# Kernel tuning notes

Measured on AMD Instinct MI355X. Metric: run time of the kernel, lower is better.

## Reference

```python
import jax, jax.numpy as jnp
import numpy as np

N_NODES = 100000
N_EDGES = 1600000
N_GRAPHS = 64
NUM_FEATURES = 512
NUM_CLASSES = 10


def setup_inputs() -> dict:
    key = jax.random.key(0)
    ks = jax.random.split(key, 8)
    x = jax.random.normal(ks[0], (N_NODES, NUM_FEATURES), dtype=jnp.float32)
    edge_index = jax.random.randint(ks[1], (2, N_EDGES), 0, N_NODES, dtype=jnp.int32)
    batch = jnp.sort(jax.random.randint(ks[2], (N_NODES,), 0, N_GRAPHS, dtype=jnp.int32))
    def init_w(k, fin, fout):
        return jax.random.normal(k, (fin, fout), dtype=jnp.float32) * (1.0 / np.sqrt(fin))
    W1 = init_w(ks[3], NUM_FEATURES, 128)
    W2 = init_w(ks[4], 128, 64)
    W3 = init_w(ks[5], 64, 32)
    Wfc = init_w(ks[6], 32, NUM_CLASSES)
    return {
        "x": x, "edge_index": edge_index, "batch": batch,
        "W1": W1, "b1": jnp.zeros((128,), jnp.float32),
        "W2": W2, "b2": jnp.zeros((64,), jnp.float32),
        "W3": W3, "b3": jnp.zeros((32,), jnp.float32),
        "Wfc": Wfc, "bfc": jnp.zeros((NUM_CLASSES,), jnp.float32),
    }


def _gcn_conv(x, src, dst, norm, W, b):
    # PyG GCNConv: linear first, then normalized neighbor aggregation (with self-loops), then bias.
    h = x @ W                                   # [N, F_out]
    msg = norm[:, None] * h[src]                # gather + scale, [E+N, F_out]
    out = jnp.zeros_like(h).at[dst].add(msg)    # scatter-add to targets
    return out + b


def reference(x, edge_index, batch, W1, b1, W2, b2, W3, b3, Wfc, bfc):
    n = x.shape[0]
    loops = jnp.arange(n, dtype=edge_index.dtype)
    src = jnp.concatenate([edge_index[0], loops])  # source nodes (+ self-loops)
    dst = jnp.concatenate([edge_index[1], loops])  # target nodes (+ self-loops)
    # symmetric normalization D^{-1/2} (A+I) D^{-1/2}; degrees counted at targets
    deg = jnp.zeros((n,), x.dtype).at[dst].add(1.0)
    dinv = jnp.where(deg > 0, jax.lax.rsqrt(deg), 0.0)
    norm = dinv[src] * dinv[dst]                # [E+N]

    h = jax.nn.relu(_gcn_conv(x, src, dst, norm, W1, b1))   # dropout is identity in eval
    h = jax.nn.relu(_gcn_conv(h, src, dst, norm, W2, b2))
    h = jax.nn.relu(_gcn_conv(h, src, dst, norm, W3, b3))

    pooled = jax.ops.segment_max(h, batch, num_segments=N_GRAPHS)  # global max pool per graph
    logits = pooled @ Wfc + bfc
    return jax.nn.log_softmax(logits, axis=1)
```

## Files before the change

### kernel.cpp

```cpp
#include <hip/hip_runtime.h>
#include <hip/hip_bf16.h>


typedef __attribute__((ext_vector_type(8))) short short8;
typedef __attribute__((ext_vector_type(8))) unsigned short ushort8v;
typedef __attribute__((ext_vector_type(4))) float f32x4;

__device__ __forceinline__ unsigned short f2bf(float f) {
    __hip_bfloat16 h = __float2bfloat16(f);
    return *(unsigned short*)&h;
}
__device__ __forceinline__ float bfu2f(unsigned short u) {
    unsigned int v = ((unsigned int)u) << 16;
    return __uint_as_float(v);
}

__global__ void init_kernel(int* __restrict__ cnt, float* __restrict__ pooled, int N) {
    int i = blockIdx.x * 256 + threadIdx.x;
    if (i < N) cnt[i] = 0;
    if (i < 64 * 32) pooled[i] = 0.0f;
}

__global__ void fill_slab(const int* __restrict__ src, const int* __restrict__ dst,
                          int* __restrict__ cnt, int* __restrict__ slab, int E) {
    int e = blockIdx.x * 256 + threadIdx.x;
    if (e < E) {
        int d = dst[e];
        int pos = atomicAdd(&cnt[d], 1);
        if (pos < 64) slab[(size_t)d * 64 + pos] = src[e];
    }
}

__global__ void dinv_kernel(const int* __restrict__ cnt, float* __restrict__ dinv, int N) {
    int i = blockIdx.x * 256 + threadIdx.x;
    if (i < N) dinv[i] = rsqrtf(1.0f + (float)cnt[i]);
}

__global__ void wconv(const float* __restrict__ W, unsigned short* __restrict__ Wt,
                      int K, int N) {
    int idx = blockIdx.x * 256 + threadIdx.x;
    if (idx < N * K) {
        int n = idx / K, k = idx % K;
        Wt[idx] = f2bf(W[(size_t)k * N + n]);
    }
}

template <int NOUT, bool A_BF16>
__global__ __launch_bounds__(256) void mfma_gemm(
        const float* __restrict__ Af, const unsigned short* __restrict__ Ab,
        const unsigned short* __restrict__ Wt, const float* __restrict__ dinv,
        unsigned short* __restrict__ C, int M, int K) {
    constexpr int NT = NOUT / 16;
    constexpr int CH = 136;

    __shared__ short As[16 * CH];
    __shared__ short Bs[NT * 4 * CH];

    const int t = threadIdx.x;
    const int w = t >> 6;
    const int lane = t & 63;
    const int row0 = blockIdx.x * 64;

    f32x4 acc[NT];
#pragma unroll
    for (int c = 0; c < NT; ++c) acc[c] = (f32x4){0.f, 0.f, 0.f, 0.f};

    const int ar = t >> 2;
    const int aq = t & 3;
    const int arow = row0 + ar;
    const int a_lds = ((ar >> 4) * 4 + aq) * CH + (ar & 15) * 8;

    const int bn = t >> 1;
    const int bh = t & 1;
    const int b_lds0 = ((bn >> 4) * 4 + 2 * bh) * CH + (bn & 15) * 8;

    for (int k0 = 0; k0 < K; k0 += 32) {
        short8 apack;
        if (A_BF16) {
            if (arow < M) apack = *(const short8*)&Ab[(size_t)arow * K + k0 + aq * 8];
            else apack = (short8){0, 0, 0, 0, 0, 0, 0, 0};
        } else {
            float4 u0 = make_float4(0.f, 0.f, 0.f, 0.f), u1 = u0;
            if (arow < M) {
                const float* ap = Af + (size_t)arow * K + k0 + aq * 8;
                u0 = *(const float4*)ap;
                u1 = *(const float4*)(ap + 4);
            }
            apack[0] = (short)f2bf(u0.x); apack[1] = (short)f2bf(u0.y);
            apack[2] = (short)f2bf(u0.z); apack[3] = (short)f2bf(u0.w);
            apack[4] = (short)f2bf(u1.x); apack[5] = (short)f2bf(u1.y);
            apack[6] = (short)f2bf(u1.z); apack[7] = (short)f2bf(u1.w);
        }
        short8 w0, w1;
        if (t < 2 * NOUT) {
            const unsigned short* wp = Wt + (size_t)bn * K + k0 + 16 * bh;
            w0 = *(const short8*)wp;
            w1 = *(const short8*)(wp + 8);
        }
        __syncthreads();
        *(short8*)&As[a_lds] = apack;
        if (t < 2 * NOUT) {
            *(short8*)&Bs[b_lds0] = w0;
            *(short8*)&Bs[b_lds0 + CH] = w1;
        }
        __syncthreads();

        short8 a = *(short8*)&As[(w * 4 + (lane >> 4)) * CH + (lane & 15) * 8];
#pragma unroll
        for (int c = 0; c < NT; ++c) {
            short8 b = *(short8*)&Bs[(c * 4 + (lane >> 4)) * CH + (lane & 15) * 8];
            acc[c] = __builtin_amdgcn_mfma_f32_16x16x32_bf16(a, b, acc[c], 0, 0, 0);
        }
    }

    const int q = lane >> 4, i = lane & 15;
#pragma unroll
    for (int reg = 0; reg < 4; ++reg) {
        int row = row0 + w * 16 + q * 4 + reg;
        if (row < M) {
            float di = dinv[row];
#pragma unroll
            for (int c = 0; c < NT; ++c)
                C[(size_t)row * NOUT + c * 16 + i] = f2bf(di * acc[c][reg]);
        }
    }
}

template <int F, bool OUT_BF16>
__global__ void gather_relu(const int* __restrict__ cnt, const int* __restrict__ slab,
                            const float* __restrict__ dinv,
                            const unsigned short* __restrict__ hs,
                            const float* __restrict__ bias, void* __restrict__ outv, int N) {
    constexpr int F8 = F / 8;
    constexpr int NPB = 256 / F8;
    const int node = blockIdx.x * NPB + threadIdx.x / F8;
    if (node >= N) return;
    const int lane = threadIdx.x % F8;
    const size_t fo = (size_t)lane * 8;

    float acc[8];
    {
        ushort8v s = *(const ushort8v*)&hs[(size_t)node * F + fo];
#pragma unroll
        for (int i = 0; i < 8; ++i) acc[i] = bfu2f(s[i]);
    }
    const int deg = cnt[node];
    const int* sl = slab + (size_t)node * 64;

    int j = 0;
    for (; j + 4 <= deg; j += 4) {
        int4 s4 = *(const int4*)&sl[j];
        ushort8v v0 = *(const ushort8v*)&hs[(size_t)s4.x * F + fo];
        ushort8v v1 = *(const ushort8v*)&hs[(size_t)s4.y * F + fo];
        ushort8v v2 = *(const ushort8v*)&hs[(size_t)s4.z * F + fo];
        ushort8v v3 = *(const ushort8v*)&hs[(size_t)s4.w * F + fo];
#pragma unroll
        for (int i = 0; i < 8; ++i)
            acc[i] += (bfu2f(v0[i]) + bfu2f(v1[i])) + (bfu2f(v2[i]) + bfu2f(v3[i]));
    }
    for (; j < deg; ++j) {
        int s = sl[j];
        ushort8v v = *(const ushort8v*)&hs[(size_t)s * F + fo];
#pragma unroll
        for (int i = 0; i < 8; ++i) acc[i] += bfu2f(v[i]);
    }

    const float di = dinv[node];
    if (OUT_BF16) {
        ushort8v o;
#pragma unroll
        for (int i = 0; i < 8; ++i) o[i] = f2bf(fmaxf(di * acc[i] + bias[fo + i], 0.f));
        *(ushort8v*)&((unsigned short*)outv)[(size_t)node * F + fo] = o;
    } else {
        float ov[8];
#pragma unroll
        for (int i = 0; i < 8; ++i) ov[i] = fmaxf(di * acc[i] + bias[fo + i], 0.f);
        float4* op = (float4*)&((float*)outv)[(size_t)node * F + fo];
        op[0] = make_float4(ov[0], ov[1], ov[2], ov[3]);
        op[1] = make_float4(ov[4], ov[5], ov[6], ov[7]);
    }
}

__global__ void pool_max(const float* __restrict__ h, const int* __restrict__ batch,
                         float* __restrict__ pooled, int N) {
    int t = blockIdx.x * 256 + threadIdx.x;
    int f = t % 32;
    int i0 = (t / 32) * 32;
    if (i0 >= N) return;
    int gcur = -1;
    float vmax = 0.f;
    for (int j = 0; j < 32; ++j) {
        int i = i0 + j;
        if (i >= N) break;
        int g = batch[i];
        if (g != gcur) {
            if (gcur >= 0) atomicMax((int*)&pooled[gcur * 32 + f], __float_as_int(vmax));
            gcur = g;
            vmax = 0.f;
        }
        vmax = fmaxf(vmax, h[(size_t)i * 32 + f]);
    }
    if (gcur >= 0) atomicMax((int*)&pooled[gcur * 32 + f], __float_as_int(vmax));
}

__global__ void head_kernel(const float* __restrict__ pooled, const float* __restrict__ Wfc,
                            const float* __restrict__ bfc, float* __restrict__ out) {
    int g = threadIdx.x;
    float p[32];
#pragma unroll
    for (int f = 0; f < 32; ++f) p[f] = pooled[g * 32 + f];
    float logits[10];
#pragma unroll
    for (int c = 0; c < 10; ++c) {
        float acc = bfc[c];
#pragma unroll
        for (int f = 0; f < 32; ++f) acc += p[f] * Wfc[f * 10 + c];
        logits[c] = acc;
    }
    float m = logits[0];
#pragma unroll
    for (int c = 1; c < 10; ++c) m = fmaxf(m, logits[c]);
    float s = 0.f;
#pragma unroll
    for (int c = 0; c < 10; ++c) s += expf(logits[c] - m);
    float lse = m + logf(s);
#pragma unroll
    for (int c = 0; c < 10; ++c) out[g * 10 + c] = logits[c] - lse;
}

extern "C" void kernel_launch(void* const* d_in, const int* in_sizes, int n_in,
                              void* d_out, int out_size, void* d_ws, size_t ws_size,
                              hipStream_t stream) {
    const float* x   = (const float*)d_in[0];
    const int*   ei  = (const int*)d_in[1];
    const int*   bat = (const int*)d_in[2];
    const float* W1  = (const float*)d_in[3];
    const float* b1  = (const float*)d_in[4];
    const float* W2  = (const float*)d_in[5];
    const float* b2  = (const float*)d_in[6];
    const float* W3  = (const float*)d_in[7];
    const float* b3  = (const float*)d_in[8];
    const float* Wfc = (const float*)d_in[9];
    const float* bfc = (const float*)d_in[10];
    float* out = (float*)d_out;

    const int N = in_sizes[2];
    const int E = in_sizes[1] / 2;
    const int K0 = in_sizes[0] / N;

    const int* src = ei;
    const int* dst = ei + E;

    float* ws = (float*)d_ws;
    float* dinv = ws;
    unsigned short* HS  = (unsigned short*)(ws + N);
    unsigned short* ACT = HS + (size_t)N * 128;
    float* H3 = (float*)ACT;
    float* pooled = (float*)(ACT + (size_t)N * 128);
    unsigned short* Wt1 = (unsigned short*)(pooled + 2048);
    unsigned short* Wt2 = Wt1 + 128 * 512;
    unsigned short* Wt3 = Wt2 + 64 * 128;
    int* iws = (int*)(Wt3 + 32 * 64);
    int* cnt = iws;
    int* slab = cnt + N;

    const int nb = (N + 255) / 256;
    const int eb = (E + 255) / 256;
    const int gb = (N + 63) / 64;

    init_kernel<<<nb, 256, 0, stream>>>(cnt, pooled, N);
    fill_slab<<<eb, 256, 0, stream>>>(src, dst, cnt, slab, E);
    dinv_kernel<<<nb, 256, 0, stream>>>(cnt, dinv, N);

    wconv<<<(128 * 512 + 255) / 256, 256, 0, stream>>>(W1, Wt1, K0, 128);
    wconv<<<(64 * 128 + 255) / 256, 256, 0, stream>>>(W2, Wt2, 128, 64);
    wconv<<<(32 * 64 + 255) / 256, 256, 0, stream>>>(W3, Wt3, 64, 32);

    const int gath128 = (N + 15) / 16;
    const int gath64  = (N + 31) / 32;
    const int gath32  = (N + 63) / 64;

    mfma_gemm<128, false><<<gb, 256, 0, stream>>>(x, nullptr, Wt1, dinv, HS, N, K0);
    gather_relu<128, true><<<gath128, 256, 0, stream>>>(cnt, slab, dinv, HS, b1, ACT, N);

    mfma_gemm<64, true><<<gb, 256, 0, stream>>>(nullptr, ACT, Wt2, dinv, HS, N, 128);
    gather_relu<64, true><<<gath64, 256, 0, stream>>>(cnt, slab, dinv, HS, b2, ACT, N);

    mfma_gemm<32, true><<<gb, 256, 0, stream>>>(nullptr, ACT, Wt3, dinv, HS, N, 64);
    gather_relu<32, false><<<gath32, 256, 0, stream>>>(cnt, slab, dinv, HS, b3, H3, N);

    pool_max<<<(((N + 31) / 32) * 32 + 255) / 256, 256, 0, stream>>>(H3, bat, pooled, N);
    head_kernel<<<1, 64, 0, stream>>>(pooled, Wfc, bfc, out);
}
```

Baseline: 603.5 us.

## Overlap first GEMM with edge slab fill in one interleaved launch

Merges the layer-1 GEMM and the edge bucketing (atomic slab fill) into a single kernel whose blocks alternate between GEMM and fill work. The two are independent, so the memory-bound GEMM and the atomic-heavy fill can run concurrently. Because dinv is not yet known when the GEMM runs, layer-1 normalization moves into the first gather, which now reads dinv per neighbour. The gather also gains an 8-wide unrolled loop and clamps degree to 64. The cost is extra dinv loads and multiplies in the layer-1 gather and some block-scheduling imbalance between the two kinds of work.

```diff
diff --git a/kernel.cpp b/kernel.cpp
--- a/kernel.cpp
+++ b/kernel.cpp
@@ -19,16 +19,6 @@
     int i = blockIdx.x * 256 + threadIdx.x;
     if (i < N) cnt[i] = 0;
     if (i < 64 * 32) pooled[i] = 0.0f;
-}
-
-__global__ void fill_slab(const int* __restrict__ src, const int* __restrict__ dst,
-                          int* __restrict__ cnt, int* __restrict__ slab, int E) {
-    int e = blockIdx.x * 256 + threadIdx.x;
-    if (e < E) {
-        int d = dst[e];
-        int pos = atomicAdd(&cnt[d], 1);
-        if (pos < 64) slab[(size_t)d * 64 + pos] = src[e];
-    }
 }
 
 __global__ void dinv_kernel(const int* __restrict__ cnt, float* __restrict__ dinv, int N) {
@@ -45,8 +35,9 @@
     }
 }
 
-template <int NOUT, bool A_BF16>
-__global__ __launch_bounds__(256) void mfma_gemm(
+template <int NOUT, bool A_BF16, bool SCALE>
+__device__ __forceinline__ void gemm_body(
+        int bid,
         const float* __restrict__ Af, const unsigned short* __restrict__ Ab,
         const unsigned short* __restrict__ Wt, const float* __restrict__ dinv,
         unsigned short* __restrict__ C, int M, int K) {
@@ -59,7 +50,7 @@
     const int t = threadIdx.x;
     const int w = t >> 6;
     const int lane = t & 63;
-    const int row0 = blockIdx.x * 64;
+    const int row0 = bid * 64;
 
     f32x4 acc[NT];
 #pragma unroll
@@ -118,7 +109,7 @@
     for (int reg = 0; reg < 4; ++reg) {
         int row = row0 + w * 16 + q * 4 + reg;
         if (row < M) {
-            float di = dinv[row];
+            float di = SCALE ? dinv[row] : 1.0f;
 #pragma unroll
             for (int c = 0; c < NT; ++c)
                 C[(size_t)row * NOUT + c * 16 + i] = f2bf(di * acc[c][reg]);
@@ -126,7 +117,57 @@
     }
 }
 
-template <int F, bool OUT_BF16>
+template <int NOUT, bool A_BF16>
+__global__ __launch_bounds__(256) void mfma_gemm(
+        const float* __restrict__ Af, const unsigned short* __restrict__ Ab,
+        const unsigned short* __restrict__ Wt, const float* __restrict__ dinv,
+        unsigned short* __restrict__ C, int M, int K) {
+    gemm_body<NOUT, A_BF16, true>(blockIdx.x, Af, Ab, Wt, dinv, C, M, K);
+}
+
+__global__ __launch_bounds__(256) void gemm1_fill(
+        const float* __restrict__ x, const unsigned short* __restrict__ Wt,
+        unsigned short* __restrict__ C, int M, int K,
+        const int* __restrict__ src, const int* __restrict__ dst,
+        int* __restrict__ cnt, int* __restrict__ slab, int E,
+        int gb, int fb) {
+    const int bx = blockIdx.x;
+    const int m = gb < fb ? gb : fb;
+    bool isg;
+    int bid;
+    if (bx < 2 * m) {
+        isg = (bx & 1) == 0;
+        bid = bx >> 1;
+    } else {
+        bid = bx - m;
+        isg = (gb > fb);
+    }
+    if (isg) {
+        gemm_body<128, false, false>(bid, x, nullptr, Wt, nullptr, C, M, K);
+    } else {
+        int e0 = bid * 1024 + (int)threadIdx.x * 4;
+        if (e0 + 4 <= E) {
+            int d0 = dst[e0], d1 = dst[e0 + 1], d2 = dst[e0 + 2], d3 = dst[e0 + 3];
+            int s0 = src[e0], s1 = src[e0 + 1], s2 = src[e0 + 2], s3 = src[e0 + 3];
+            int p0 = atomicAdd(&cnt[d0], 1);
+            int p1 = atomicAdd(&cnt[d1], 1);
+            int p2 = atomicAdd(&cnt[d2], 1);
+            int p3 = atomicAdd(&cnt[d3], 1);
+            if (p0 < 64) slab[(size_t)d0 * 64 + p0] = s0;
+            if (p1 < 64) slab[(size_t)d1 * 64 + p1] = s1;
+            if (p2 < 64) slab[(size_t)d2 * 64 + p2] = s2;
+            if (p3 < 64) slab[(size_t)d3 * 64 + p3] = s3;
+        } else {
+            for (int e = e0; e < E; ++e) {
+                int d = dst[e];
+                int p = atomicAdd(&cnt[d], 1);
+                if (p < 64) slab[(size_t)d * 64 + p] = src[e];
+            }
+        }
+    }
+}
+
+template <int F, bool OUT_BF16, bool PRESCALED>
 __global__ void gather_relu(const int* __restrict__ cnt, const int* __restrict__ slab,
                             const float* __restrict__ dinv,
                             const unsigned short* __restrict__ hs,
@@ -137,35 +178,76 @@
     if (node >= N) return;
     const int lane = threadIdx.x % F8;
     const size_t fo = (size_t)lane * 8;
+    const float di = dinv[node];
 
     float acc[8];
     {
         ushort8v s = *(const ushort8v*)&hs[(size_t)node * F + fo];
 #pragma unroll
-        for (int i = 0; i < 8; ++i) acc[i] = bfu2f(s[i]);
-    }
-    const int deg = cnt[node];
+        for (int i = 0; i < 8; ++i) acc[i] = PRESCALED ? bfu2f(s[i]) : di * bfu2f(s[i]);
+    }
+    int deg = cnt[node];
+    if (deg > 64) deg = 64;
     const int* sl = slab + (size_t)node * 64;
 
     int j = 0;
+    for (; j + 8 <= deg; j += 8) {
+        int4 a4 = *(const int4*)&sl[j];
+        int4 b4 = *(const int4*)&sl[j + 4];
+        ushort8v v0 = *(const ushort8v*)&hs[(size_t)a4.x * F + fo];
+        ushort8v v1 = *(const ushort8v*)&hs[(size_t)a4.y * F + fo];
+        ushort8v v2 = *(const ushort8v*)&hs[(size_t)a4.z * F + fo];
+        ushort8v v3 = *(const ushort8v*)&hs[(size_t)a4.w * F + fo];
+        ushort8v v4 = *(const ushort8v*)&hs[(size_t)b4.x * F + fo];
+        ushort8v v5 = *(const ushort8v*)&hs[(size_t)b4.y * F + fo];
+        ushort8v v6 = *(const ushort8v*)&hs[(size_t)b4.z * F + fo];
+        ushort8v v7 = *(const ushort8v*)&hs[(size_t)b4.w * F + fo];
+        if (PRESCALED) {
+#pragma unroll
+            for (int i = 0; i < 8; ++i)
+                acc[i] += ((bfu2f(v0[i]) + bfu2f(v1[i])) + (bfu2f(v2[i]) + bfu2f(v3[i]))) +
+                          ((bfu2f(v4[i]) + bfu2f(v5[i])) + (bfu2f(v6[i]) + bfu2f(v7[i])));
+        } else {
+            float w0 = dinv[a4.x], w1 = dinv[a4.y], w2 = dinv[a4.z], w3 = dinv[a4.w];
+            float w4 = dinv[b4.x], w5 = dinv[b4.y], w6 = dinv[b4.z], w7 = dinv[b4.w];
+#pragma unroll
+            for (int i = 0; i < 8; ++i) {
+                float s01 = fmaf(w0, bfu2f(v0[i]), w1 * bfu2f(v1[i]));
+                float s23 = fmaf(w2, bfu2f(v2[i]), w3 * bfu2f(v3[i]));
+                float s45 = fmaf(w4, bfu2f(v4[i]), w5 * bfu2f(v5[i]));
+                float s67 = fmaf(w6, bfu2f(v6[i]), w7 * bfu2f(v7[i]));
+                acc[i] += (s01 + s23) + (s45 + s67);
+            }
+        }
+    }
     for (; j + 4 <= deg; j += 4) {
         int4 s4 = *(const int4*)&sl[j];
         ushort8v v0 = *(const ushort8v*)&hs[(size_t)s4.x * F + fo];
         ushort8v v1 = *(const ushort8v*)&hs[(size_t)s4.y * F + fo];
         ushort8v v2 = *(const ushort8v*)&hs[(size_t)s4.z * F + fo];
         ushort8v v3 = *(const ushort8v*)&hs[(size_t)s4.w * F + fo];
-#pragma unroll
-        for (int i = 0; i < 8; ++i)
-            acc[i] += (bfu2f(v0[i]) + bfu2f(v1[i])) + (bfu2f(v2[i]) + bfu2f(v3[i]));
+        if (PRESCALED) {
+#pragma unroll
+            for (int i = 0; i < 8; ++i)
+                acc[i] += (bfu2f(v0[i]) + bfu2f(v1[i])) + (bfu2f(v2[i]) + bfu2f(v3[i]));
+        } else {
+            float w0 = dinv[s4.x], w1 = dinv[s4.y], w2 = dinv[s4.z], w3 = dinv[s4.w];
+#pragma unroll
+            for (int i = 0; i < 8; ++i) {
+                float s01 = fmaf(w0, bfu2f(v0[i]), w1 * bfu2f(v1[i]));
+                float s23 = fmaf(w2, bfu2f(v2[i]), w3 * bfu2f(v3[i]));
+                acc[i] += s01 + s23;
+            }
+        }
     }
     for (; j < deg; ++j) {
         int s = sl[j];
         ushort8v v = *(const ushort8v*)&hs[(size_t)s * F + fo];
-#pragma unroll
-        for (int i = 0; i < 8; ++i) acc[i] += bfu2f(v[i]);
-    }
-
-    const float di = dinv[node];
+        float w = PRESCALED ? 1.0f : dinv[s];
+#pragma unroll
+        for (int i = 0; i < 8; ++i) acc[i] = fmaf(w, bfu2f(v[i]), acc[i]);
+    }
+
     if (OUT_BF16) {
         ushort8v o;
 #pragma unroll
@@ -265,13 +347,10 @@
     int* slab = cnt + N;
 
     const int nb = (N + 255) / 256;
-    const int eb = (E + 255) / 256;
     const int gb = (N + 63) / 64;
+    const int fb = (E + 1023) / 1024;
 
     init_kernel<<<nb, 256, 0, stream>>>(cnt, pooled, N);
-    fill_slab<<<eb, 256, 0, stream>>>(src, dst, cnt, slab, E);
-    dinv_kernel<<<nb, 256, 0, stream>>>(cnt, dinv, N);
-
     wconv<<<(128 * 512 + 255) / 256, 256, 0, stream>>>(W1, Wt1, K0, 128);
     wconv<<<(64 * 128 + 255) / 256, 256, 0, stream>>>(W2, Wt2, 128, 64);
     wconv<<<(32 * 64 + 255) / 256, 256, 0, stream>>>(W3, Wt3, 64, 32);
@@ -280,14 +359,16 @@
     const int gath64  = (N + 31) / 32;
     const int gath32  = (N + 63) / 64;
 
-    mfma_gemm<128, false><<<gb, 256, 0, stream>>>(x, nullptr, Wt1, dinv, HS, N, K0);
-    gather_relu<128, true><<<gath128, 256, 0, stream>>>(cnt, slab, dinv, HS, b1, ACT, N);
+    gemm1_fill<<<gb + fb, 256, 0, stream>>>(x, Wt1, HS, N, K0,
+                                            src, dst, cnt, slab, E, gb, fb);
+    dinv_kernel<<<nb, 256, 0, stream>>>(cnt, dinv, N);
+    gather_relu<128, true, false><<<gath128, 256, 0, stream>>>(cnt, slab, dinv, HS, b1, ACT, N);
 
     mfma_gemm<64, true><<<gb, 256, 0, stream>>>(nullptr, ACT, Wt2, dinv, HS, N, 128);
-    gather_relu<64, true><<<gath64, 256, 0, stream>>>(cnt, slab, dinv, HS, b2, ACT, N);
+    gather_relu<64, true, true><<<gath64, 256, 0, stream>>>(cnt, slab, dinv, HS, b2, ACT, N);
 
     mfma_gemm<32, true><<<gb, 256, 0, stream>>>(nullptr, ACT, Wt3, dinv, HS, N, 64);
-    gather_relu<32, false><<<gath32, 256, 0, stream>>>(cnt, slab, dinv, HS, b3, H3, N);
+    gather_relu<32, false, true><<<gath32, 256, 0, stream>>>(cnt, slab, dinv, HS, b3, H3, N);
 
     pool_max<<<(((N + 31) / 32) * 32 + 255) / 256, 256, 0, stream>>>(H3, bat, pooled, N);
     head_kernel<<<1, 64, 0, stream>>>(pooled, Wfc, bfc, out);
```

Result: faster. 547.0 us (-9.4%).

## Build CSR slab via two-pass bucketed edge partition instead of global atomics

Applied to the files above, without the earlier changes.

Replaces the per-edge global atomicAdd slab fill with two passes. First, edges are binned into 128-node buckets with shared-memory histograms and scans. Second, each bucket is turned into the per-node slab in LDS and written out coalesced, with degrees and dinv computed in the same kernel. The gather also gets an 8-wide unrolled neighbor loop and clamps degree at 64. The aim is to remove scattered global atomics and random writes, at the cost of extra kernels and fixed bucket capacity limits (CAPB) that could drop edges in skewed graphs.

```diff
diff --git a/kernel.cpp b/kernel.cpp
--- a/kernel.cpp
+++ b/kernel.cpp
@@ -6,6 +6,10 @@
 typedef __attribute__((ext_vector_type(8))) unsigned short ushort8v;
 typedef __attribute__((ext_vector_type(4))) float f32x4;
 
+constexpr int NB   = 1024;
+constexpr int CAPB = 4096;
+constexpr int EPB  = 6400;
+
 __device__ __forceinline__ unsigned short f2bf(float f) {
     __hip_bfloat16 h = __float2bfloat16(f);
     return *(unsigned short*)&h;
@@ -15,25 +19,109 @@
     return __uint_as_float(v);
 }
 
-__global__ void init_kernel(int* __restrict__ cnt, float* __restrict__ pooled, int N) {
+__global__ void init_kernel(int* __restrict__ bcnt, float* __restrict__ pooled) {
     int i = blockIdx.x * 256 + threadIdx.x;
-    if (i < N) cnt[i] = 0;
+    if (i < NB * 16) bcnt[i] = 0;
     if (i < 64 * 32) pooled[i] = 0.0f;
 }
 
-__global__ void fill_slab(const int* __restrict__ src, const int* __restrict__ dst,
-                          int* __restrict__ cnt, int* __restrict__ slab, int E) {
-    int e = blockIdx.x * 256 + threadIdx.x;
-    if (e < E) {
-        int d = dst[e];
-        int pos = atomicAdd(&cnt[d], 1);
-        if (pos < 64) slab[(size_t)d * 64 + pos] = src[e];
-    }
-}
-
-__global__ void dinv_kernel(const int* __restrict__ cnt, float* __restrict__ dinv, int N) {
-    int i = blockIdx.x * 256 + threadIdx.x;
-    if (i < N) dinv[i] = rsqrtf(1.0f + (float)cnt[i]);
+__global__ __launch_bounds__(256) void partition_edges(
+        const int* __restrict__ src, const int* __restrict__ dst,
+        int* __restrict__ bcnt, unsigned* __restrict__ bucketed, int E) {
+    __shared__ unsigned h[NB], rs[NB], cur[NB], gs[NB];
+    __shared__ unsigned wtot[4];
+    __shared__ unsigned ebuf[EPB];
+    __shared__ unsigned short ebkt[EPB];
+
+    const int t = threadIdx.x;
+    const int e0 = blockIdx.x * EPB;
+    const int nloc = min(EPB, E - e0);
+
+    for (int i = t; i < NB; i += 256) h[i] = 0;
+    __syncthreads();
+
+    for (int i = t; i < nloc; i += 256) {
+        int d = dst[e0 + i];
+        atomicAdd(&h[d >> 7], 1u);
+    }
+    __syncthreads();
+
+    const unsigned b0 = 4u * t;
+    unsigned s0 = h[b0], s1 = h[b0 + 1], s2 = h[b0 + 2], s3 = h[b0 + 3];
+    unsigned tsum = s0 + s1 + s2 + s3;
+    unsigned scan = tsum;
+#pragma unroll
+    for (int off = 1; off < 64; off <<= 1) {
+        unsigned v = __shfl_up(scan, off, 64);
+        if ((t & 63) >= off) scan += v;
+    }
+    if ((t & 63) == 63) wtot[t >> 6] = scan;
+    __syncthreads();
+    unsigned woff = 0;
+    for (int w = 0; w < (t >> 6); ++w) woff += wtot[w];
+    unsigned excl = woff + scan - tsum;
+    rs[b0] = excl;                 cur[b0] = excl;
+    rs[b0 + 1] = excl + s0;        cur[b0 + 1] = excl + s0;
+    rs[b0 + 2] = excl + s0 + s1;   cur[b0 + 2] = excl + s0 + s1;
+    rs[b0 + 3] = excl + s0 + s1 + s2; cur[b0 + 3] = excl + s0 + s1 + s2;
+    if (s0) gs[b0]     = (unsigned)atomicAdd(&bcnt[(b0) * 16], (int)s0);
+    if (s1) gs[b0 + 1] = (unsigned)atomicAdd(&bcnt[(b0 + 1) * 16], (int)s1);
+    if (s2) gs[b0 + 2] = (unsigned)atomicAdd(&bcnt[(b0 + 2) * 16], (int)s2);
+    if (s3) gs[b0 + 3] = (unsigned)atomicAdd(&bcnt[(b0 + 3) * 16], (int)s3);
+    __syncthreads();
+
+    for (int i = t; i < nloc; i += 256) {
+        int d = dst[e0 + i];
+        int s = src[e0 + i];
+        int b = d >> 7;
+        unsigned p = atomicAdd(&cur[b], 1u);
+        ebuf[p] = ((unsigned)s << 7) | (unsigned)(d & 127);
+        ebkt[p] = (unsigned short)b;
+    }
+    __syncthreads();
+
+    for (int p = t; p < nloc; p += 256) {
+        unsigned v = ebuf[p];
+        int b = ebkt[p];
+        unsigned g = gs[b] + ((unsigned)p - rs[b]);
+        if (g < CAPB) bucketed[(size_t)b * CAPB + g] = v;
+    }
+}
+
+__global__ __launch_bounds__(256) void bucket_csr(
+        const unsigned* __restrict__ bucketed, const int* __restrict__ bcnt,
+        int* __restrict__ cnt, int* __restrict__ slab, float* __restrict__ dinv, int N) {
+    __shared__ int lcnt[128];
+    __shared__ unsigned lslab[128 * 64];
+
+    const int b = blockIdx.x;
+    const int t = threadIdx.x;
+    if (t < 128) lcnt[t] = 0;
+    __syncthreads();
+
+    int nE = bcnt[b * 16];
+    if (nE > CAPB) nE = CAPB;
+    const unsigned* bb = bucketed + (size_t)b * CAPB;
+    for (int e = t; e < nE; e += 256) {
+        unsigned v = bb[e];
+        int ln = v & 127;
+        int pos = atomicAdd(&lcnt[ln], 1);
+        if (pos < 64) lslab[ln * 64 + pos] = v >> 7;
+    }
+    __syncthreads();
+
+    const int node0 = b * 128;
+    const int nnodes = min(128, N - node0);
+    if (nnodes <= 0) return;
+    const int tot4 = (nnodes * 64) / 4;
+    int4* gout = (int4*)&slab[(size_t)node0 * 64];
+    const int4* lin = (const int4*)lslab;
+    for (int i = t; i < tot4; i += 256) gout[i] = lin[i];
+    if (t < nnodes) {
+        int deg = lcnt[t];
+        cnt[node0 + t] = deg;
+        dinv[node0 + t] = rsqrtf(1.0f + (float)deg);
+    }
 }
 
 __global__ void wconv(const float* __restrict__ W, unsigned short* __restrict__ Wt,
@@ -144,10 +232,27 @@
 #pragma unroll
         for (int i = 0; i < 8; ++i) acc[i] = bfu2f(s[i]);
     }
-    const int deg = cnt[node];
+    int deg = cnt[node];
+    if (deg > 64) deg = 64;
     const int* sl = slab + (size_t)node * 64;
 
     int j = 0;
+    for (; j + 8 <= deg; j += 8) {
+        int4 a4 = *(const int4*)&sl[j];
+        int4 b4 = *(const int4*)&sl[j + 4];
+        ushort8v v0 = *(const ushort8v*)&hs[(size_t)a4.x * F + fo];
+        ushort8v v1 = *(const ushort8v*)&hs[(size_t)a4.y * F + fo];
+        ushort8v v2 = *(const ushort8v*)&hs[(size_t)a4.z * F + fo];
+        ushort8v v3 = *(const ushort8v*)&hs[(size_t)a4.w * F + fo];
+        ushort8v v4 = *(const ushort8v*)&hs[(size_t)b4.x * F + fo];
+        ushort8v v5 = *(const ushort8v*)&hs[(size_t)b4.y * F + fo];
+        ushort8v v6 = *(const ushort8v*)&hs[(size_t)b4.z * F + fo];
+        ushort8v v7 = *(const ushort8v*)&hs[(size_t)b4.w * F + fo];
+#pragma unroll
+        for (int i = 0; i < 8; ++i)
+            acc[i] += ((bfu2f(v0[i]) + bfu2f(v1[i])) + (bfu2f(v2[i]) + bfu2f(v3[i]))) +
+                      ((bfu2f(v4[i]) + bfu2f(v5[i])) + (bfu2f(v6[i]) + bfu2f(v7[i])));
+    }
     for (; j + 4 <= deg; j += 4) {
         int4 s4 = *(const int4*)&sl[j];
         ushort8v v0 = *(const ushort8v*)&hs[(size_t)s4.x * F + fo];
@@ -260,22 +365,22 @@
     unsigned short* Wt1 = (unsigned short*)(pooled + 2048);
     unsigned short* Wt2 = Wt1 + 128 * 512;
     unsigned short* Wt3 = Wt2 + 64 * 128;
-    int* iws = (int*)(Wt3 + 32 * 64);
-    int* cnt = iws;
+    int* cnt = (int*)(Wt3 + 32 * 64);
     int* slab = cnt + N;
-
-    const int nb = (N + 255) / 256;
-    const int eb = (E + 255) / 256;
+    int* bcnt = slab + (size_t)N * 64;
+    unsigned* bucketed = (unsigned*)(bcnt + NB * 16);
+
     const int gb = (N + 63) / 64;
-
-    init_kernel<<<nb, 256, 0, stream>>>(cnt, pooled, N);
-    fill_slab<<<eb, 256, 0, stream>>>(src, dst, cnt, slab, E);
-    dinv_kernel<<<nb, 256, 0, stream>>>(cnt, dinv, N);
-
+    const int NBUCK = (N + 127) >> 7;
+
+    init_kernel<<<64, 256, 0, stream>>>(bcnt, pooled);
     wconv<<<(128 * 512 + 255) / 256, 256, 0, stream>>>(W1, Wt1, K0, 128);
     wconv<<<(64 * 128 + 255) / 256, 256, 0, stream>>>(W2, Wt2, 128, 64);
     wconv<<<(32 * 64 + 255) / 256, 256, 0, stream>>>(W3, Wt3, 64, 32);
 
+    partition_edges<<<(E + EPB - 1) / EPB, 256, 0, stream>>>(src, dst, bcnt, bucketed, E);
+    bucket_csr<<<NBUCK, 256, 0, stream>>>(bucketed, bcnt, cnt, slab, dinv, N);
+
     const int gath128 = (N + 15) / 16;
     const int gath64  = (N + 31) / 32;
     const int gath32  = (N + 63) / 64;
```

Measured after the change: 533.9 us. 11.5% less time.
